# Optimization experiments

Measured on AMD Instinct MI355X. Metric: run time of the kernel, lower is better.

The kernel has to match this reference:

```python
import jax, jax.numpy as jnp
import numpy as np

N = 100000
EPS_BN = 1e-5


def setup_inputs() -> dict:
    key = jax.random.key(0)
    ks = jax.random.split(key, 12)
    x = jax.random.normal(ks[0], (N, 128), dtype=jnp.float32)
    edge_index = jax.random.randint(ks[1], (2, 800000), 0, N, dtype=jnp.int64)
    # GCNConv layer params (PyG: lin weight [out,in], bias added after aggregation)
    s = 1.0 / np.sqrt(128.0)
    W1 = jax.random.uniform(ks[2], (128, 128), jnp.float32, -s, s)
    b1 = jnp.zeros((128,), jnp.float32)
    W2 = jax.random.uniform(ks[3], (128, 128), jnp.float32, -s, s)
    b2 = jnp.zeros((128,), jnp.float32)
    # BatchNorm affine params
    g1 = jnp.ones((128,), jnp.float32)
    be1 = jnp.zeros((128,), jnp.float32)
    g2 = jnp.ones((128,), jnp.float32)
    be2 = jnp.zeros((128,), jnp.float32)
    # PReLU single shared parameter (torch init = 0.25)
    a = jnp.asarray(0.25, jnp.float32)
    return {"x": x, "edge_index": edge_index, "W1": W1, "b1": b1, "g1": g1,
            "be1": be1, "W2": W2, "b2": b2, "g2": g2, "be2": be2, "a": a}


def _gcn_conv(x, src, dst, deg_inv_sqrt, W, b):
    # x' = D^-1/2 (A+I) D^-1/2 (x W^T) + b  (self loops already in src/dst)
    h = x @ W.T                                   # [N, out]
    norm = deg_inv_sqrt[src] * deg_inv_sqrt[dst]  # [E+N]
    msg = h[src] * norm[:, None]                  # gather + scale
    out = jax.ops.segment_sum(msg, dst, num_segments=N)  # scatter-add
    return out + b


def _batchnorm(x, g, be):
    # training-mode BatchNorm1d over nodes (biased variance)
    mean = jnp.mean(x, axis=0)
    var = jnp.mean(jnp.square(x - mean), axis=0)
    return (x - mean) * jax.lax.rsqrt(var + EPS_BN) * g + be


def _prelu(x, a):
    return jnp.where(x > 0, x, a * x)


def reference(x, edge_index, W1, b1, g1, be1, W2, b2, g2, be2, a):
    # add self loops
    loops = jnp.arange(N, dtype=edge_index.dtype)
    src = jnp.concatenate([edge_index[0], loops])
    dst = jnp.concatenate([edge_index[1], loops])
    # symmetric normalization from in-degree at destinations
    deg = jax.ops.segment_sum(jnp.ones_like(dst, dtype=x.dtype), dst, num_segments=N)
    deg_inv_sqrt = jnp.where(deg > 0, jax.lax.rsqrt(deg), 0.0)

    h = _gcn_conv(x, src, dst, deg_inv_sqrt, W1, b1)
    h = _prelu(_batchnorm(h, g1, be1), a)
    h = _gcn_conv(h, src, dst, deg_inv_sqrt, W2, b2)
    h = _prelu(_batchnorm(h, g2, be2), a)
    return h
```

## Files before the change

kernel.cpp:

```cpp
#include <hip/hip_runtime.h>
#include <cstddef>
#include <cstdint>


#define EPS_BN 1e-5f
#define BN_BLOCKS 256

typedef short short8 __attribute__((ext_vector_type(8)));
typedef float f32x4 __attribute__((ext_vector_type(4)));

static __device__ __forceinline__ unsigned short f2b(float f) {
    union { float f; uint32_t u; } v; v.f = f;
    uint32_t u = v.u;
    return (unsigned short)((u + 0x7FFFu + ((u >> 16) & 1u)) >> 16);
}
static __device__ __forceinline__ float b2f(unsigned short h) {
    union { uint32_t u; float f; } v; v.u = ((uint32_t)h) << 16;
    return v.f;
}
static __device__ __forceinline__ float b2f_s(short h) { return b2f((unsigned short)h); }

__global__ __launch_bounds__(256) void k_prep(const float* __restrict__ W1, const float* __restrict__ W2,
                                              unsigned short* __restrict__ Wz1, unsigned short* __restrict__ Wz2,
                                              const int* __restrict__ dst, int* __restrict__ cnt,
                                              int* __restrict__ rank, int E) {
    int bid = blockIdx.x, tid = threadIdx.x;
    if (bid < 128) {
        int gi = bid * 256 + tid;
        const float* W = (gi < 16384) ? W1 : W2;
        unsigned short* Wz = (gi < 16384) ? Wz1 : Wz2;
        int idx = gi & 16383;
        int o = idx >> 7, k = idx & 127;
        int ct = o >> 4, nn = o & 15, ks = k >> 5, q = (k >> 3) & 3, j = k & 7;
        Wz[(ct * 4 + ks) * 512 + (q * 16 + nn) * 8 + j] = f2b(W[idx]);
    } else {
        int e = (bid - 128) * 256 + tid;
        if (e < E) rank[e] = atomicAdd(&cnt[dst[e]], 1);
    }
}

__global__ __launch_bounds__(256) void k_scanA(const int* __restrict__ cnt, int* __restrict__ partial, int n) {
    __shared__ int sd[256];
    int tid = threadIdx.x;
    int base = blockIdx.x * 1024 + tid * 4;
    int s = 0;
#pragma unroll
    for (int j = 0; j < 4; j++) { int idx = base + j; if (idx < n) s += cnt[idx]; }
    sd[tid] = s; __syncthreads();
    for (int off = 128; off > 0; off >>= 1) {
        if (tid < off) sd[tid] += sd[tid + off];
        __syncthreads();
    }
    if (tid == 0) partial[blockIdx.x] = sd[0];
}

__global__ __launch_bounds__(256) void k_scanC(const int* __restrict__ cnt, const int* __restrict__ partial,
                                               int* __restrict__ rowptr, float* __restrict__ dis, int n, int nb) {
    __shared__ int sp[256];
    __shared__ int sd[256];
    int tid = threadIdx.x;
    sp[tid] = (tid < nb) ? partial[tid] : 0;
    int base = blockIdx.x * 1024 + tid * 4;
    int v[4]; int s = 0;
#pragma unroll
    for (int j = 0; j < 4; j++) { int idx = base + j; v[j] = (idx < n) ? cnt[idx] : 0; s += v[j]; }
    sd[tid] = s;
    __syncthreads();
    for (int off = 1; off < 256; off <<= 1) {
        int a = (tid >= off) ? sp[tid - off] : 0;
        int b = (tid >= off) ? sd[tid - off] : 0;
        __syncthreads();
        sp[tid] += a; sd[tid] += b;
        __syncthreads();
    }
    int gbase = (blockIdx.x == 0) ? 0 : sp[blockIdx.x - 1];
    int excl = gbase + ((tid == 0) ? 0 : sd[tid - 1]);
#pragma unroll
    for (int j = 0; j < 4; j++) {
        int idx = base + j;
        if (idx < n) {
            rowptr[idx] = excl;
            dis[idx] = rsqrtf((float)(v[j] + 1));
        }
        excl += v[j];
    }
}

__global__ __launch_bounds__(256) void k_fill_gemm1(const float* __restrict__ X,
                                                    const unsigned short* __restrict__ Wz,
                                                    unsigned short* __restrict__ Yb, int n,
                                                    const int* __restrict__ src, const int* __restrict__ dst,
                                                    const int* __restrict__ rowptr, const int* __restrict__ rank,
                                                    int* __restrict__ colw, int E, int gGemm) {
    __shared__ unsigned short lds[16384];
    int tid = threadIdx.x;
    if ((int)blockIdx.x >= gGemm) {
        int e = (blockIdx.x - gGemm) * 256 + tid;
        if (e < E) {
            int d = dst[e];
            colw[rowptr[d] + rank[e]] = src[e];
        }
        return;
    }
    const short8* wsrc = (const short8*)Wz;
    short8* ldst = (short8*)lds;
#pragma unroll
    for (int i = 0; i < 8; i++) ldst[tid + 256 * i] = wsrc[tid + 256 * i];
    __syncthreads();

    int wave = tid >> 6, lane = tid & 63;
    int r0 = blockIdx.x * 64 + wave * 16;
    int mrow = lane & 15, quad = lane >> 4;
    int arow = r0 + mrow; if (arow > n - 1) arow = n - 1;
    const float* xr = X + (size_t)arow * 128;

    f32x4 acc[8];
#pragma unroll
    for (int ct = 0; ct < 8; ct++) acc[ct] = (f32x4){0.f, 0.f, 0.f, 0.f};

#pragma unroll
    for (int ks = 0; ks < 4; ks++) {
        int kb = ks * 32 + quad * 8;
        float4 x0 = *reinterpret_cast<const float4*>(xr + kb);
        float4 x1 = *reinterpret_cast<const float4*>(xr + kb + 4);
        short8 a;
        a[0] = (short)f2b(x0.x); a[1] = (short)f2b(x0.y); a[2] = (short)f2b(x0.z); a[3] = (short)f2b(x0.w);
        a[4] = (short)f2b(x1.x); a[5] = (short)f2b(x1.y); a[6] = (short)f2b(x1.z); a[7] = (short)f2b(x1.w);
#pragma unroll
        for (int ct = 0; ct < 8; ct++) {
            short8 b = *(const short8*)(lds + (ct * 4 + ks) * 512 + lane * 8);
            acc[ct] = __builtin_amdgcn_mfma_f32_16x16x32_bf16(a, b, acc[ct], 0, 0, 0);
        }
    }
#pragma unroll
    for (int i = 0; i < 4; i++) {
        int row = r0 + quad * 4 + i;
        if (row < n) {
#pragma unroll
            for (int ct = 0; ct < 8; ct++)
                Yb[(size_t)row * 128 + ct * 16 + mrow] = f2b(acc[ct][i]);
        }
    }
}

__global__ __launch_bounds__(256) void k_gemm2(const unsigned short* __restrict__ Ab,
                                               const unsigned short* __restrict__ Wz,
                                               const float* __restrict__ sc, const float* __restrict__ sh,
                                               const float* __restrict__ ap,
                                               unsigned short* __restrict__ Yb, int n) {
    __shared__ unsigned short lds[16384];
    int tid = threadIdx.x;
    const short8* wsrc = (const short8*)Wz;
    short8* ldst = (short8*)lds;
#pragma unroll
    for (int i = 0; i < 8; i++) ldst[tid + 256 * i] = wsrc[tid + 256 * i];
    __syncthreads();

    float alpha = ap[0];
    int wave = tid >> 6, lane = tid & 63;
    int r0 = blockIdx.x * 64 + wave * 16;
    int mrow = lane & 15, quad = lane >> 4;
    int arow = r0 + mrow; if (arow > n - 1) arow = n - 1;
    const unsigned short* ar = Ab + (size_t)arow * 128;

    f32x4 acc[8];
#pragma unroll
    for (int ct = 0; ct < 8; ct++) acc[ct] = (f32x4){0.f, 0.f, 0.f, 0.f};

#pragma unroll
    for (int ks = 0; ks < 4; ks++) {
        int kb = ks * 32 + quad * 8;
        short8 raw = *(const short8*)(ar + kb);
        float4 s0 = *reinterpret_cast<const float4*>(sc + kb);
        float4 s1 = *reinterpret_cast<const float4*>(sc + kb + 4);
        float4 t0 = *reinterpret_cast<const float4*>(sh + kb);
        float4 t1 = *reinterpret_cast<const float4*>(sh + kb + 4);
        float ss[8] = {s0.x, s0.y, s0.z, s0.w, s1.x, s1.y, s1.z, s1.w};
        float tt[8] = {t0.x, t0.y, t0.z, t0.w, t1.x, t1.y, t1.z, t1.w};
        short8 a;
#pragma unroll
        for (int j = 0; j < 8; j++) {
            float x = fmaf(b2f_s(raw[j]), ss[j], tt[j]);
            x = x > 0.f ? x : alpha * x;
            a[j] = (short)f2b(x);
        }
#pragma unroll
        for (int ct = 0; ct < 8; ct++) {
            short8 b = *(const short8*)(lds + (ct * 4 + ks) * 512 + lane * 8);
            acc[ct] = __builtin_amdgcn_mfma_f32_16x16x32_bf16(a, b, acc[ct], 0, 0, 0);
        }
    }
#pragma unroll
    for (int i = 0; i < 4; i++) {
        int row = r0 + quad * 4 + i;
        if (row < n) {
#pragma unroll
            for (int ct = 0; ct < 8; ct++)
                Yb[(size_t)row * 128 + ct * 16 + mrow] = f2b(acc[ct][i]);
        }
    }
}

__global__ __launch_bounds__(256) void k_agg(const unsigned short* __restrict__ Hb,
                                             const int* __restrict__ rowptr, const int* __restrict__ cnt,
                                             const int* __restrict__ colw, const float* __restrict__ dis,
                                             const float* __restrict__ bias,
                                             unsigned short* __restrict__ outb, int n) {
    int lane = threadIdx.x & 15;
    int node = blockIdx.x * 16 + (threadIdx.x >> 4);
    if (node >= n) return;
    int lo = lane * 8;
    float dn = dis[node];
    short8 hv = *(const short8*)(Hb + (size_t)node * 128 + lo);
    float acc[8];
#pragma unroll
    for (int j = 0; j < 8; j++) acc[j] = dn * b2f_s(hv[j]);
    int num = cnt[node];
    int beg = rowptr[node];
    const int* cw = colw + beg;
    int e = 0;
    for (; e + 4 <= num; e += 4) {
        int s0 = cw[e], s1 = cw[e + 1], s2 = cw[e + 2], s3 = cw[e + 3];
        float w0 = dis[s0], w1 = dis[s1], w2 = dis[s2], w3 = dis[s3];
        short8 n0 = *(const short8*)(Hb + (size_t)s0 * 128 + lo);
        short8 n1 = *(const short8*)(Hb + (size_t)s1 * 128 + lo);
        short8 n2 = *(const short8*)(Hb + (size_t)s2 * 128 + lo);
        short8 n3 = *(const short8*)(Hb + (size_t)s3 * 128 + lo);
#pragma unroll
        for (int j = 0; j < 8; j++) {
            acc[j] = fmaf(w0, b2f_s(n0[j]), acc[j]);
            acc[j] = fmaf(w1, b2f_s(n1[j]), acc[j]);
            acc[j] = fmaf(w2, b2f_s(n2[j]), acc[j]);
            acc[j] = fmaf(w3, b2f_s(n3[j]), acc[j]);
        }
    }
    for (; e < num; ++e) {
        int s = cw[e];
        float w = dis[s];
        short8 nb = *(const short8*)(Hb + (size_t)s * 128 + lo);
#pragma unroll
        for (int j = 0; j < 8; j++) acc[j] = fmaf(w, b2f_s(nb[j]), acc[j]);
    }
    const float4 bv0 = reinterpret_cast<const float4*>(bias)[lane * 2 + 0];
    const float4 bv1 = reinterpret_cast<const float4*>(bias)[lane * 2 + 1];
    float bb[8] = {bv0.x, bv0.y, bv0.z, bv0.w, bv1.x, bv1.y, bv1.z, bv1.w};
    short8 ov;
#pragma unroll
    for (int j = 0; j < 8; j++) ov[j] = (short)f2b(fmaf(dn, acc[j], bb[j]));
    *(short8*)(outb + (size_t)node * 128 + lo) = ov;
}

__global__ __launch_bounds__(256) void k_bnstats(const unsigned short* __restrict__ X, float* __restrict__ part, int n) {
    __shared__ float ls[16][128];
    __shared__ float lq[16][128];
    int tid = threadIdx.x;
    int rs = tid >> 4, g = tid & 15;
    float s[8], q[8];
#pragma unroll
    for (int j = 0; j < 8; j++) { s[j] = 0.f; q[j] = 0.f; }
#pragma unroll 4
    for (int r = blockIdx.x * 16 + rs; r < n; r += BN_BLOCKS * 16) {
        short8 v = *(const short8*)(X + (size_t)r * 128 + g * 8);
#pragma unroll
        for (int j = 0; j < 8; j++) {
            float f = b2f_s(v[j]);
            s[j] += f; q[j] = fmaf(f, f, q[j]);
        }
    }
#pragma unroll
    for (int j = 0; j < 8; j++) { ls[rs][g * 8 + j] = s[j]; lq[rs][g * 8 + j] = q[j]; }
    __syncthreads();
    for (int off = 8; off > 0; off >>= 1) {
        if (rs < off) {
#pragma unroll
            for (int j = 0; j < 8; j++) {
                ls[rs][g * 8 + j] += ls[rs + off][g * 8 + j];
                lq[rs][g * 8 + j] += lq[rs + off][g * 8 + j];
            }
        }
        __syncthreads();
    }
    if (tid < 128) part[blockIdx.x * 256 + tid] = ls[0][tid];
    else           part[blockIdx.x * 256 + tid] = lq[0][tid - 128];
}

__global__ __launch_bounds__(1024) void k_bnparams(const float* __restrict__ part, const float* __restrict__ g,
                                                   const float* __restrict__ be, float* __restrict__ sc,
                                                   float* __restrict__ sh, float invN) {
    __shared__ float lsum[8][128];
    __shared__ float lsq[8][128];
    int tid = threadIdx.x;
    int f = tid & 127, c = tid >> 7;
    float s = 0.f, q = 0.f;
#pragma unroll 4
    for (int b = c * 32; b < c * 32 + 32; b++) {
        s += part[b * 256 + f];
        q += part[b * 256 + 128 + f];
    }
    lsum[c][f] = s; lsq[c][f] = q;
    __syncthreads();
    if (tid < 128) {
        float ss = 0.f, qq = 0.f;
#pragma unroll
        for (int c2 = 0; c2 < 8; c2++) { ss += lsum[c2][tid]; qq += lsq[c2][tid]; }
        float mean = ss * invN;
        float var = qq * invN - mean * mean;
        float rstd = rsqrtf(var + EPS_BN);
        float scale = g[tid] * rstd;
        sc[tid] = scale;
        sh[tid] = fmaf(-mean, scale, be[tid]);
    }
}

__global__ __launch_bounds__(256) void k_bnact_f(const unsigned short* __restrict__ X, float* __restrict__ Y,
                                                 const float* __restrict__ sc, const float* __restrict__ sh,
                                                 const float* __restrict__ ap, int n8) {
    int i = blockIdx.x * 256 + threadIdx.x;
    if (i >= n8) return;
    float a = ap[0];
    int g = i & 15;
    const float4 s0 = reinterpret_cast<const float4*>(sc)[g * 2 + 0];
    const float4 s1 = reinterpret_cast<const float4*>(sc)[g * 2 + 1];
    const float4 t0 = reinterpret_cast<const float4*>(sh)[g * 2 + 0];
    const float4 t1 = reinterpret_cast<const float4*>(sh)[g * 2 + 1];
    float ss[8] = {s0.x, s0.y, s0.z, s0.w, s1.x, s1.y, s1.z, s1.w};
    float tt[8] = {t0.x, t0.y, t0.z, t0.w, t1.x, t1.y, t1.z, t1.w};
    short8 v = reinterpret_cast<const short8*>(X)[i];
    float out[8];
#pragma unroll
    for (int j = 0; j < 8; j++) {
        float x = fmaf(b2f_s(v[j]), ss[j], tt[j]);
        out[j] = x > 0.f ? x : a * x;
    }
    float4 o0 = {out[0], out[1], out[2], out[3]};
    float4 o1 = {out[4], out[5], out[6], out[7]};
    reinterpret_cast<float4*>(Y)[i * 2 + 0] = o0;
    reinterpret_cast<float4*>(Y)[i * 2 + 1] = o1;
}

extern "C" void kernel_launch(void* const* d_in, const int* in_sizes, int n_in,
                              void* d_out, int out_size, void* d_ws, size_t ws_size,
                              hipStream_t stream) {
    (void)n_in; (void)out_size; (void)ws_size;
    const float* x   = (const float*)d_in[0];
    const int*   ei  = (const int*)d_in[1];
    const float* W1  = (const float*)d_in[2];
    const float* b1  = (const float*)d_in[3];
    const float* g1  = (const float*)d_in[4];
    const float* be1 = (const float*)d_in[5];
    const float* W2  = (const float*)d_in[6];
    const float* b2  = (const float*)d_in[7];
    const float* g2  = (const float*)d_in[8];
    const float* be2 = (const float*)d_in[9];
    const float* ap  = (const float*)d_in[10];
    float* out = (float*)d_out;

    const int N = in_sizes[0] / 128;
    const int E = in_sizes[1] / 2;
    const int* srcIdx = ei;
    const int* dstIdx = ei + E;

    char* w = (char*)d_ws;
    size_t off = 0;
    auto alloc = [&](size_t bytes) { char* p = w + off; off += (bytes + 255) & ~(size_t)255; return p; };
    int*   cnt     = (int*)  alloc((size_t)N * 4);
    int*   rowptr  = (int*)  alloc((size_t)N * 4);
    int*   rank    = (int*)  alloc((size_t)E * 4);
    int*   colw    = (int*)  alloc((size_t)E * 4);
    float* dis     = (float*)alloc((size_t)N * 4);
    int*   partial = (int*)  alloc(4096);
    float* part    = (float*)alloc((size_t)BN_BLOCKS * 256 * 4);
    float* sc1     = (float*)alloc(512);
    float* sh1     = (float*)alloc(512);
    float* sc2     = (float*)alloc(512);
    float* sh2     = (float*)alloc(512);
    unsigned short* Wz1 = (unsigned short*)alloc(16384 * 2);
    unsigned short* Wz2 = (unsigned short*)alloc(16384 * 2);
    unsigned short* bufH = (unsigned short*)alloc((size_t)N * 128 * 2);
    unsigned short* bufA = (unsigned short*)alloc((size_t)N * 128 * 2);

    const float invN = 1.0f / (float)N;
    const int NB = (N + 1023) / 1024;
    const int gE = (E + 255) / 256;
    const int n8 = N * 16;
    const int gGemm = (N + 63) / 64;
    const int gAgg  = (N + 15) / 16;

    hipMemsetAsync(cnt, 0, (size_t)N * 4, stream);

    k_prep<<<128 + gE, 256, 0, stream>>>(W1, W2, Wz1, Wz2, dstIdx, cnt, rank, E);

    k_scanA<<<NB, 256, 0, stream>>>(cnt, partial, N);
    k_scanC<<<NB, 256, 0, stream>>>(cnt, partial, rowptr, dis, N, NB);

    k_fill_gemm1<<<gGemm + gE, 256, 0, stream>>>(x, Wz1, bufH, N,
                                                 srcIdx, dstIdx, rowptr, rank, colw, E, gGemm);
    k_agg<<<gAgg, 256, 0, stream>>>(bufH, rowptr, cnt, colw, dis, b1, bufA, N);
    k_bnstats<<<BN_BLOCKS, 256, 0, stream>>>(bufA, part, N);
    k_bnparams<<<1, 1024, 0, stream>>>(part, g1, be1, sc1, sh1, invN);

    k_gemm2<<<gGemm, 256, 0, stream>>>(bufA, Wz2, sc1, sh1, ap, bufH, N);
    k_agg<<<gAgg, 256, 0, stream>>>(bufH, rowptr, cnt, colw, dis, b2, bufA, N);
    k_bnstats<<<BN_BLOCKS, 256, 0, stream>>>(bufA, part, N);
    k_bnparams<<<1, 1024, 0, stream>>>(part, g2, be2, sc2, sh2, invN);
    k_bnact_f<<<(n8 + 255) / 256, 256, 0, stream>>>(bufA, out, sc2, sh2, ap, n8);
}
```

Measured before the change: 296.7 us.

## Fuse BN statistics into aggregation and process 4 row tiles per GEMM wave

The separate batch-norm statistics kernel is removed: each aggregation block now reduces the per-feature sum and sum of squares of its 16 output nodes in shared memory and writes a partial. This saves a full re-read of the aggregated activations twice per forward. As a trade-off, k_bnparams must now reduce about 6250 partials instead of 256 in a single block, which could become a serial bottleneck. Separately, the GEMM kernels loop over 4 sub-tiles per wave, so each block covers 256 rows and amortises its weight load into LDS over four times more work.

```diff
diff --git a/kernel.cpp b/kernel.cpp
--- a/kernel.cpp
+++ b/kernel.cpp
@@ -4,7 +4,6 @@
 
 
 #define EPS_BN 1e-5f
-#define BN_BLOCKS 256
 
 typedef short short8 __attribute__((ext_vector_type(8)));
 typedef float f32x4 __attribute__((ext_vector_type(4)));
@@ -109,36 +108,40 @@
     __syncthreads();
 
     int wave = tid >> 6, lane = tid & 63;
-    int r0 = blockIdx.x * 64 + wave * 16;
     int mrow = lane & 15, quad = lane >> 4;
-    int arow = r0 + mrow; if (arow > n - 1) arow = n - 1;
-    const float* xr = X + (size_t)arow * 128;
-
-    f32x4 acc[8];
-#pragma unroll
-    for (int ct = 0; ct < 8; ct++) acc[ct] = (f32x4){0.f, 0.f, 0.f, 0.f};
-
-#pragma unroll
-    for (int ks = 0; ks < 4; ks++) {
-        int kb = ks * 32 + quad * 8;
-        float4 x0 = *reinterpret_cast<const float4*>(xr + kb);
-        float4 x1 = *reinterpret_cast<const float4*>(xr + kb + 4);
-        short8 a;
-        a[0] = (short)f2b(x0.x); a[1] = (short)f2b(x0.y); a[2] = (short)f2b(x0.z); a[3] = (short)f2b(x0.w);
-        a[4] = (short)f2b(x1.x); a[5] = (short)f2b(x1.y); a[6] = (short)f2b(x1.z); a[7] = (short)f2b(x1.w);
-#pragma unroll
-        for (int ct = 0; ct < 8; ct++) {
-            short8 b = *(const short8*)(lds + (ct * 4 + ks) * 512 + lane * 8);
-            acc[ct] = __builtin_amdgcn_mfma_f32_16x16x32_bf16(a, b, acc[ct], 0, 0, 0);
-        }
-    }
-#pragma unroll
-    for (int i = 0; i < 4; i++) {
-        int row = r0 + quad * 4 + i;
-        if (row < n) {
-#pragma unroll
-            for (int ct = 0; ct < 8; ct++)
-                Yb[(size_t)row * 128 + ct * 16 + mrow] = f2b(acc[ct][i]);
+    int r0w = blockIdx.x * 256 + wave * 64;
+
+    for (int s = 0; s < 4; ++s) {
+        int r0 = r0w + s * 16;
+        int arow = r0 + mrow; if (arow > n - 1) arow = n - 1;
+        const float* xr = X + (size_t)arow * 128;
+
+        f32x4 acc[8];
+#pragma unroll
+        for (int ct = 0; ct < 8; ct++) acc[ct] = (f32x4){0.f, 0.f, 0.f, 0.f};
+
+#pragma unroll
+        for (int ks = 0; ks < 4; ks++) {
+            int kb = ks * 32 + quad * 8;
+            float4 x0 = *reinterpret_cast<const float4*>(xr + kb);
+            float4 x1 = *reinterpret_cast<const float4*>(xr + kb + 4);
+            short8 a;
+            a[0] = (short)f2b(x0.x); a[1] = (short)f2b(x0.y); a[2] = (short)f2b(x0.z); a[3] = (short)f2b(x0.w);
+            a[4] = (short)f2b(x1.x); a[5] = (short)f2b(x1.y); a[6] = (short)f2b(x1.z); a[7] = (short)f2b(x1.w);
+#pragma unroll
+            for (int ct = 0; ct < 8; ct++) {
+                short8 b = *(const short8*)(lds + (ct * 4 + ks) * 512 + lane * 8);
+                acc[ct] = __builtin_amdgcn_mfma_f32_16x16x32_bf16(a, b, acc[ct], 0, 0, 0);
+            }
+        }
+#pragma unroll
+        for (int i = 0; i < 4; i++) {
+            int row = r0 + quad * 4 + i;
+            if (row < n) {
+#pragma unroll
+                for (int ct = 0; ct < 8; ct++)
+                    Yb[(size_t)row * 128 + ct * 16 + mrow] = f2b(acc[ct][i]);
+            }
         }
     }
 }
@@ -158,65 +161,74 @@
 
     float alpha = ap[0];
     int wave = tid >> 6, lane = tid & 63;
-    int r0 = blockIdx.x * 64 + wave * 16;
     int mrow = lane & 15, quad = lane >> 4;
-    int arow = r0 + mrow; if (arow > n - 1) arow = n - 1;
-    const unsigned short* ar = Ab + (size_t)arow * 128;
-
-    f32x4 acc[8];
-#pragma unroll
-    for (int ct = 0; ct < 8; ct++) acc[ct] = (f32x4){0.f, 0.f, 0.f, 0.f};
-
-#pragma unroll
-    for (int ks = 0; ks < 4; ks++) {
-        int kb = ks * 32 + quad * 8;
-        short8 raw = *(const short8*)(ar + kb);
-        float4 s0 = *reinterpret_cast<const float4*>(sc + kb);
-        float4 s1 = *reinterpret_cast<const float4*>(sc + kb + 4);
-        float4 t0 = *reinterpret_cast<const float4*>(sh + kb);
-        float4 t1 = *reinterpret_cast<const float4*>(sh + kb + 4);
-        float ss[8] = {s0.x, s0.y, s0.z, s0.w, s1.x, s1.y, s1.z, s1.w};
-        float tt[8] = {t0.x, t0.y, t0.z, t0.w, t1.x, t1.y, t1.z, t1.w};
-        short8 a;
-#pragma unroll
-        for (int j = 0; j < 8; j++) {
-            float x = fmaf(b2f_s(raw[j]), ss[j], tt[j]);
-            x = x > 0.f ? x : alpha * x;
-            a[j] = (short)f2b(x);
-        }
-#pragma unroll
-        for (int ct = 0; ct < 8; ct++) {
-            short8 b = *(const short8*)(lds + (ct * 4 + ks) * 512 + lane * 8);
-            acc[ct] = __builtin_amdgcn_mfma_f32_16x16x32_bf16(a, b, acc[ct], 0, 0, 0);
-        }
-    }
-#pragma unroll
-    for (int i = 0; i < 4; i++) {
-        int row = r0 + quad * 4 + i;
-        if (row < n) {
-#pragma unroll
-            for (int ct = 0; ct < 8; ct++)
-                Yb[(size_t)row * 128 + ct * 16 + mrow] = f2b(acc[ct][i]);
-        }
-    }
-}
-
-__global__ __launch_bounds__(256) void k_agg(const unsigned short* __restrict__ Hb,
-                                             const int* __restrict__ rowptr, const int* __restrict__ cnt,
-                                             const int* __restrict__ colw, const float* __restrict__ dis,
-                                             const float* __restrict__ bias,
-                                             unsigned short* __restrict__ outb, int n) {
-    int lane = threadIdx.x & 15;
-    int node = blockIdx.x * 16 + (threadIdx.x >> 4);
-    if (node >= n) return;
+    int r0w = blockIdx.x * 256 + wave * 64;
+
+    for (int s = 0; s < 4; ++s) {
+        int r0 = r0w + s * 16;
+        int arow = r0 + mrow; if (arow > n - 1) arow = n - 1;
+        const unsigned short* ar = Ab + (size_t)arow * 128;
+
+        f32x4 acc[8];
+#pragma unroll
+        for (int ct = 0; ct < 8; ct++) acc[ct] = (f32x4){0.f, 0.f, 0.f, 0.f};
+
+#pragma unroll
+        for (int ks = 0; ks < 4; ks++) {
+            int kb = ks * 32 + quad * 8;
+            short8 raw = *(const short8*)(ar + kb);
+            float4 s0 = *reinterpret_cast<const float4*>(sc + kb);
+            float4 s1 = *reinterpret_cast<const float4*>(sc + kb + 4);
+            float4 t0 = *reinterpret_cast<const float4*>(sh + kb);
+            float4 t1 = *reinterpret_cast<const float4*>(sh + kb + 4);
+            float ss[8] = {s0.x, s0.y, s0.z, s0.w, s1.x, s1.y, s1.z, s1.w};
+            float tt[8] = {t0.x, t0.y, t0.z, t0.w, t1.x, t1.y, t1.z, t1.w};
+            short8 a;
+#pragma unroll
+            for (int j = 0; j < 8; j++) {
+                float x = fmaf(b2f_s(raw[j]), ss[j], tt[j]);
+                x = x > 0.f ? x : alpha * x;
+                a[j] = (short)f2b(x);
+            }
+#pragma unroll
+            for (int ct = 0; ct < 8; ct++) {
+                short8 b = *(const short8*)(lds + (ct * 4 + ks) * 512 + lane * 8);
+                acc[ct] = __builtin_amdgcn_mfma_f32_16x16x32_bf16(a, b, acc[ct], 0, 0, 0);
+            }
+        }
+#pragma unroll
+        for (int i = 0; i < 4; i++) {
+            int row = r0 + quad * 4 + i;
+            if (row < n) {
+#pragma unroll
+                for (int ct = 0; ct < 8; ct++)
+                    Yb[(size_t)row * 128 + ct * 16 + mrow] = f2b(acc[ct][i]);
+            }
+        }
+    }
+}
+
+__global__ __launch_bounds__(256) void k_aggst(const unsigned short* __restrict__ Hb,
+                                               const int* __restrict__ rowptr, const int* __restrict__ cnt,
+                                               const int* __restrict__ colw, const float* __restrict__ dis,
+                                               const float* __restrict__ bias,
+                                               unsigned short* __restrict__ outb,
+                                               float* __restrict__ part, int n) {
+    __shared__ float ls[16][128];
+    __shared__ float lq[16][128];
+    int tid = threadIdx.x;
+    int lane = tid & 15, slot = tid >> 4;
+    int node = blockIdx.x * 16 + slot;
+    bool act = node < n;
+    int nodec = act ? node : (n - 1);
     int lo = lane * 8;
-    float dn = dis[node];
-    short8 hv = *(const short8*)(Hb + (size_t)node * 128 + lo);
+    float dn = dis[nodec];
+    short8 hv = *(const short8*)(Hb + (size_t)nodec * 128 + lo);
     float acc[8];
 #pragma unroll
     for (int j = 0; j < 8; j++) acc[j] = dn * b2f_s(hv[j]);
-    int num = cnt[node];
-    int beg = rowptr[node];
+    int num = act ? cnt[nodec] : 0;
+    int beg = rowptr[nodec];
     const int* cw = colw + beg;
     int e = 0;
     for (; e + 4 <= num; e += 4) {
@@ -245,57 +257,46 @@
     const float4 bv1 = reinterpret_cast<const float4*>(bias)[lane * 2 + 1];
     float bb[8] = {bv0.x, bv0.y, bv0.z, bv0.w, bv1.x, bv1.y, bv1.z, bv1.w};
     short8 ov;
-#pragma unroll
-    for (int j = 0; j < 8; j++) ov[j] = (short)f2b(fmaf(dn, acc[j], bb[j]));
-    *(short8*)(outb + (size_t)node * 128 + lo) = ov;
-}
-
-__global__ __launch_bounds__(256) void k_bnstats(const unsigned short* __restrict__ X, float* __restrict__ part, int n) {
-    __shared__ float ls[16][128];
-    __shared__ float lq[16][128];
-    int tid = threadIdx.x;
-    int rs = tid >> 4, g = tid & 15;
-    float s[8], q[8];
-#pragma unroll
-    for (int j = 0; j < 8; j++) { s[j] = 0.f; q[j] = 0.f; }
-#pragma unroll 4
-    for (int r = blockIdx.x * 16 + rs; r < n; r += BN_BLOCKS * 16) {
-        short8 v = *(const short8*)(X + (size_t)r * 128 + g * 8);
-#pragma unroll
-        for (int j = 0; j < 8; j++) {
-            float f = b2f_s(v[j]);
-            s[j] += f; q[j] = fmaf(f, f, q[j]);
-        }
-    }
-#pragma unroll
-    for (int j = 0; j < 8; j++) { ls[rs][g * 8 + j] = s[j]; lq[rs][g * 8 + j] = q[j]; }
+    float fv[8];
+#pragma unroll
+    for (int j = 0; j < 8; j++) {
+        float y = fmaf(dn, acc[j], bb[j]);
+        unsigned short h = f2b(y);
+        ov[j] = (short)h;
+        fv[j] = act ? b2f(h) : 0.f;
+    }
+    if (act) *(short8*)(outb + (size_t)node * 128 + lo) = ov;
+#pragma unroll
+    for (int j = 0; j < 8; j++) {
+        ls[slot][lane * 8 + j] = fv[j];
+        lq[slot][lane * 8 + j] = fv[j] * fv[j];
+    }
     __syncthreads();
     for (int off = 8; off > 0; off >>= 1) {
-        if (rs < off) {
+        if (slot < off) {
 #pragma unroll
             for (int j = 0; j < 8; j++) {
-                ls[rs][g * 8 + j] += ls[rs + off][g * 8 + j];
-                lq[rs][g * 8 + j] += lq[rs + off][g * 8 + j];
+                ls[slot][lane * 8 + j] += ls[slot + off][lane * 8 + j];
+                lq[slot][lane * 8 + j] += lq[slot + off][lane * 8 + j];
             }
         }
         __syncthreads();
     }
-    if (tid < 128) part[blockIdx.x * 256 + tid] = ls[0][tid];
-    else           part[blockIdx.x * 256 + tid] = lq[0][tid - 128];
+    if (tid < 128) part[(size_t)blockIdx.x * 256 + tid] = ls[0][tid];
+    else           part[(size_t)blockIdx.x * 256 + tid] = lq[0][tid - 128];
 }
 
 __global__ __launch_bounds__(1024) void k_bnparams(const float* __restrict__ part, const float* __restrict__ g,
                                                    const float* __restrict__ be, float* __restrict__ sc,
-                                                   float* __restrict__ sh, float invN) {
+                                                   float* __restrict__ sh, float invN, int nb) {
     __shared__ float lsum[8][128];
     __shared__ float lsq[8][128];
     int tid = threadIdx.x;
     int f = tid & 127, c = tid >> 7;
     float s = 0.f, q = 0.f;
-#pragma unroll 4
-    for (int b = c * 32; b < c * 32 + 32; b++) {
-        s += part[b * 256 + f];
-        q += part[b * 256 + 128 + f];
+    for (int b = c; b < nb; b += 8) {
+        s += part[(size_t)b * 256 + f];
+        q += part[(size_t)b * 256 + 128 + f];
     }
     lsum[c][f] = s; lsq[c][f] = q;
     __syncthreads();
@@ -360,6 +361,12 @@
     const int* srcIdx = ei;
     const int* dstIdx = ei + E;
 
+    const int NB = (N + 1023) / 1024;
+    const int gE = (E + 255) / 256;
+    const int n8 = N * 16;
+    const int gGemm = (N + 255) / 256;
+    const int gAgg  = (N + 15) / 16;
+
     char* w = (char*)d_ws;
     size_t off = 0;
     auto alloc = [&](size_t bytes) { char* p = w + off; off += (bytes + 255) & ~(size_t)255; return p; };
@@ -369,7 +376,7 @@
     int*   colw    = (int*)  alloc((size_t)E * 4);
     float* dis     = (float*)alloc((size_t)N * 4);
     int*   partial = (int*)  alloc(4096);
-    float* part    = (float*)alloc((size_t)BN_BLOCKS * 256 * 4);
+    float* part    = (float*)alloc((size_t)gAgg * 256 * 4);
     float* sc1     = (float*)alloc(512);
     float* sh1     = (float*)alloc(512);
     float* sc2     = (float*)alloc(512);
@@ -380,11 +387,6 @@
     unsigned short* bufA = (unsigned short*)alloc((size_t)N * 128 * 2);
 
     const float invN = 1.0f / (float)N;
-    const int NB = (N + 1023) / 1024;
-    const int gE = (E + 255) / 256;
-    const int n8 = N * 16;
-    const int gGemm = (N + 63) / 64;
-    const int gAgg  = (N + 15) / 16;
 
     hipMemsetAsync(cnt, 0, (size_t)N * 4, stream);
 
@@ -395,13 +397,11 @@
 
     k_fill_gemm1<<<gGemm + gE, 256, 0, stream>>>(x, Wz1, bufH, N,
                                                  srcIdx, dstIdx, rowptr, rank, colw, E, gGemm);
-    k_agg<<<gAgg, 256, 0, stream>>>(bufH, rowptr, cnt, colw, dis, b1, bufA, N);
-    k_bnstats<<<BN_BLOCKS, 256, 0, stream>>>(bufA, part, N);
-    k_bnparams<<<1, 1024, 0, stream>>>(part, g1, be1, sc1, sh1, invN);
+    k_aggst<<<gAgg, 256, 0, stream>>>(bufH, rowptr, cnt, colw, dis, b1, bufA, part, N);
+    k_bnparams<<<1, 1024, 0, stream>>>(part, g1, be1, sc1, sh1, invN, gAgg);
 
     k_gemm2<<<gGemm, 256, 0, stream>>>(bufA, Wz2, sc1, sh1, ap, bufH, N);
-    k_agg<<<gAgg, 256, 0, stream>>>(bufH, rowptr, cnt, colw, dis, b2, bufA, N);
-    k_bnstats<<<BN_BLOCKS, 256, 0, stream>>>(bufA, part, N);
-    k_bnparams<<<1, 1024, 0, stream>>>(part, g2, be2, sc2, sh2, invN);
+    k_aggst<<<gAgg, 256, 0, stream>>>(bufH, rowptr, cnt, colw, dis, b2, bufA, part, N);
+    k_bnparams<<<1, 1024, 0, stream>>>(part, g2, be2, sc2, sh2, invN, gAgg);
     k_bnact_f<<<(n8 + 255) / 256, 256, 0, stream>>>(bufA, out, sc2, sh2, ap, n8);
 }
```

New measurement: 744.7 us. 151% more time.
